# Performance work log

Hardware: AMD Instinct MI355X
Metric: run time of the kernel (lower is better)

Reference implementation:

```python
import jax, jax.numpy as jnp
import numpy as np
from jax import lax

N_CLASS = 21
K_ED = 5
ALPHA = 0.1
BN_EPS = 1e-5


def _conv(x, w):
    # NCHW conv, stride 1, SAME padding
    return lax.conv_general_dilated(x, w, (1, 1), 'SAME',
                                    dimension_numbers=('NCHW', 'OIHW', 'NCHW'))


def _bn(x, g, b, m, v):
    # inference-mode BatchNorm2d with running stats
    scale = (g * lax.rsqrt(v + BN_EPS))[None, :, None, None]
    return (x - m[None, :, None, None]) * scale + b[None, :, None, None]


def _maxpool(x, k):
    return lax.reduce_window(x, -jnp.inf, lax.max, (1, 1, k, k), (1, 1, 1, 1), 'SAME')


def setup_inputs() -> dict:
    key = jax.random.key(0)
    ks = jax.random.split(key, 12)
    N, F, H, W, C = 8, 512, 96, 96, N_CLASS
    feature = jax.random.normal(ks[0], (N, F, H, W), jnp.float32)
    global_pred = jax.random.normal(ks[1], (N, C, H, W), jnp.float32)
    conv1_w = jax.random.normal(ks[2], (256, F, 3, 3), jnp.float32) * 0.02
    bn1_g = jnp.ones((256,), jnp.float32)
    bn1_b = jnp.zeros((256,), jnp.float32)
    bn1_m = jax.random.normal(ks[3], (256,), jnp.float32) * 0.1
    bn1_v = jax.random.uniform(ks[4], (256,), jnp.float32, 0.5, 1.5)
    conv2_w = jax.random.normal(ks[5], (128, 256, 3, 3), jnp.float32) * 0.02
    bn2_g = jnp.ones((128,), jnp.float32)
    bn2_b = jnp.zeros((128,), jnp.float32)
    bn2_m = jax.random.normal(ks[6], (128,), jnp.float32) * 0.1
    bn2_v = jax.random.uniform(ks[7], (128,), jnp.float32, 0.5, 1.5)
    conv3_w = jax.random.normal(ks[8], (C, 128, 1, 1), jnp.float32) * 0.02
    conv3_b = jnp.zeros((C,), jnp.float32)
    return dict(feature=feature, global_pred=global_pred,
                conv1_w=conv1_w, bn1_g=bn1_g, bn1_b=bn1_b, bn1_m=bn1_m, bn1_v=bn1_v,
                conv2_w=conv2_w, bn2_g=bn2_g, bn2_b=bn2_b, bn2_m=bn2_m, bn2_v=bn2_v,
                conv3_w=conv3_w, conv3_b=conv3_b)


def reference(feature, global_pred, conv1_w, bn1_g, bn1_b, bn1_m, bn1_v,
              conv2_w, bn2_g, bn2_b, bn2_m, bn2_v, conv3_w, conv3_b):
    N, F, H, W = feature.shape
    # hard labels -> one-hot [N, C, H, W]
    lbl = jnp.argmax(global_pred, axis=1)
    onehot = jnp.transpose(jax.nn.one_hot(lbl, N_CLASS, dtype=feature.dtype), (0, 3, 1, 2))
    # binary morphology: dilation = max-pool, erosion = -max-pool(-x)
    d = _maxpool(onehot, K_ED)
    e = -_maxpool(-onehot, K_ED)
    transition = jnp.sum(d - e, axis=1, keepdims=True)
    transition = jnp.where(transition >= 1.0, 1.0, transition)  # [N,1,H,W]
    tfeat = feature * transition
    # per-class masked mean over ALL H*W pixels (faithful to .mean(dim=2))
    objs = jnp.einsum('nfhw,nchw->ncf', feature, e) / (H * W)  # [N,C,F]
    # cdist(p=2) between transition-feature pixels and class prototypes
    x = tfeat.reshape(N, F, H * W).transpose(0, 2, 1)  # [N,HW,F]
    x2 = jnp.sum(x * x, axis=-1, keepdims=True)
    o2 = jnp.sum(objs * objs, axis=-1)
    d2 = jnp.maximum(x2 + o2[:, None, :] - 2.0 * jnp.einsum('npf,ncf->npc', x, objs), 0.0)
    cd = jnp.where(d2 > 0, jnp.sqrt(jnp.where(d2 > 0, d2, 1.0)), 0.0)  # safe sqrt
    dist = 1.0 - jax.nn.softmax(cd, axis=-1)  # [N,HW,C]
    obj_feat = jnp.einsum('npc,ncf->nfp', dist, objs).reshape(N, F, H, W)
    fusion = (feature * (1.0 - transition)
              + feature * transition * ALPHA
              + obj_feat * transition * (1.0 - ALPHA))
    # fusion_predictor: convBNReLU -> bilinear x2 -> convBNReLU -> 1x1 conv
    h = jax.nn.relu(_bn(_conv(fusion, conv1_w), bn1_g, bn1_b, bn1_m, bn1_v))
    h = jax.image.resize(h, (N, 256, 2 * H, 2 * W), method='bilinear')
    h = jax.nn.relu(_bn(_conv(h, conv2_w), bn2_g, bn2_b, bn2_m, bn2_v))
    logits = _conv(h, conv3_w) + conv3_b[None, :, None, None]
    # eval mode: softmax over classes
    return jax.nn.softmax(logits, axis=1)
```

## Files before the change

### kernel.cpp

```cpp
#include <hip/hip_runtime.h>
#include <cstdint>
#include <cstddef>

typedef __attribute__((ext_vector_type(4))) float f32x4;
typedef __attribute__((ext_vector_type(8))) short short8;

__device__ __forceinline__ float bf2f(unsigned short u) {
  union { unsigned int i; float f; } x; x.i = ((unsigned int)u) << 16; return x.f;
}
__device__ __forceinline__ unsigned short f2bf(float f) {
  union { float f; unsigned int i; } x; x.f = f;
  unsigned int r = x.i + 0x7fffu + ((x.i >> 16) & 1u);
  return (unsigned short)(r >> 16);
}
__device__ __forceinline__ void gload16(unsigned short* lds, const unsigned short* g) {
  __builtin_amdgcn_global_load_lds(
      (const __attribute__((address_space(1))) unsigned int*)g,
      (__attribute__((address_space(3))) unsigned int*)lds, 16, 0, 0);
}

__global__ void k_prepbn(const float* __restrict__ g1, const float* __restrict__ b1,
                         const float* __restrict__ m1, const float* __restrict__ v1,
                         const float* __restrict__ g2, const float* __restrict__ b2,
                         const float* __restrict__ m2, const float* __restrict__ v2,
                         float* __restrict__ s1, float* __restrict__ bb1,
                         float* __restrict__ s2, float* __restrict__ bb2) {
  int i = threadIdx.x;
  if (i < 256) { float s = g1[i] * rsqrtf(v1[i] + 1e-5f); s1[i] = s; bb1[i] = b1[i] - m1[i] * s; }
  if (i < 128) { float s = g2[i] * rsqrtf(v2[i] + 1e-5f); s2[i] = s; bb2[i] = b2[i] - m2[i] * s; }
}

__global__ void k_prepw1(const float* __restrict__ w, unsigned short* __restrict__ wt) {
  int i = blockIdx.x * 256 + threadIdx.x;
  int o = i / 4608, k = i - o * 4608;
  int cblk = k / 288, r = k - cblk * 288;
  int t = r >> 5, cl = r & 31;
  int ci = cblk * 32 + cl;
  int ty = t / 3, tx = t - ty * 3;
  wt[i] = f2bf(w[((o * 512 + ci) * 3 + ty) * 3 + tx]);
}
__global__ void k_prepw2(const float* __restrict__ w, unsigned short* __restrict__ wt) {
  int i = blockIdx.x * 256 + threadIdx.x;
  int o = i / 2304, k = i - o * 2304;
  int cblk = k / 288, r = k - cblk * 288;
  int t = r >> 5, cl = r & 31;
  int ci = cblk * 32 + cl;
  int ty = t / 3, tx = t - ty * 3;
  wt[i] = f2bf(w[((o * 256 + ci) * 3 + ty) * 3 + tx]);
}
__global__ void k_prepw3(const float* __restrict__ w3, unsigned short* __restrict__ w3b) {
  int i = blockIdx.x * 256 + threadIdx.x;
  int c = i >> 7, k = i & 127;
  w3b[i] = (c < 21) ? f2bf(w3[c * 128 + k]) : (unsigned short)0;
}

template <int HP, int WP, int C>
__global__ void k_border(unsigned short* __restrict__ p) {
  const int B = 2 * WP + 2 * (HP - 2);
  const int total = 8 * B * (C / 8);
  int i = blockIdx.x * 256 + threadIdx.x;
  if (i >= total) return;
  const int cg = i % (C / 8);
  int b = i / (C / 8);
  const int n = b / B; b -= n * B;
  int y, x;
  if (b < WP) { y = 0; x = b; }
  else if (b < 2 * WP) { y = HP - 1; x = b - WP; }
  else { int r = b - 2 * WP; y = 1 + (r >> 1); x = (r & 1) ? (WP - 1) : 0; }
  short8 z = {0, 0, 0, 0, 0, 0, 0, 0};
  *(short8*)&p[(((long)n * HP + y) * WP + x) * C + cg * 8] = z;
}

__global__ __launch_bounds__(256)
void k_featT(const float* __restrict__ feat, unsigned short* __restrict__ featT) {
  const int g = blockIdx.x * 256 + threadIdx.x;
  const int n = g / 9216, p = g - n * 9216;
  const int fg0 = blockIdx.y * 16;
  const float* src = feat + (long)n * 512 * 9216 + p;
  unsigned short* dst = featT + ((long)n * 9216 + p) * 512;
  for (int fg = fg0; fg < fg0 + 16; fg++) {
    short8 o;
    #pragma unroll
    for (int j = 0; j < 8; j++) o[j] = (short)f2bf(src[(long)(fg * 8 + j) * 9216]);
    *(short8*)&dst[fg * 8] = o;
  }
}

__global__ void k_labels(const float* __restrict__ gp, signed char* __restrict__ lab) {
  int p = blockIdx.x * 256 + threadIdx.x;
  int n = p / 9216, q = p - n * 9216;
  const float* g = gp + (long)n * 21 * 9216 + q;
  float best = g[0]; int bi = 0;
  #pragma unroll
  for (int c = 1; c < 21; c++) {
    float v = g[(long)c * 9216];
    if (v > best) { best = v; bi = c; }
  }
  lab[p] = (signed char)bi;
}

__global__ void k_em(const signed char* __restrict__ lab, signed char* __restrict__ em) {
  int p = blockIdx.x * 256 + threadIdx.x;
  int n = p / 9216, q = p - n * 9216, y = q / 96, x = q - y * 96;
  const signed char* L = lab + n * 9216;
  signed char l0 = L[q];
  bool uni = true;
  for (int dy = -2; dy <= 2; dy++) {
    int yy = y + dy; if (yy < 0 || yy > 95) continue;
    for (int dx = -2; dx <= 2; dx++) {
      int xx = x + dx; if (xx < 0 || xx > 95) continue;
      uni = uni && (L[yy * 96 + xx] == l0);
    }
  }
  em[p] = uni ? l0 : (signed char)-1;
}

__global__ void k_objs(const float* __restrict__ feat, const signed char* __restrict__ em,
                       float* __restrict__ objs) {
  const int n = blockIdx.y;
  const int wv = threadIdx.x >> 6, lane = threadIdx.x & 63;
  const int f = blockIdx.x * 4 + wv;
  const float* src = feat + ((long)n * 512 + f) * 9216;
  const signed char* e = em + n * 9216;
  float a[21];
  #pragma unroll
  for (int c = 0; c < 21; c++) a[c] = 0.f;
  for (int p = lane; p < 9216; p += 64) {
    float v = src[p];
    int c0 = e[p];
    #pragma unroll
    for (int c = 0; c < 21; c++) a[c] += (c0 == c) ? v : 0.f;
  }
  #pragma unroll
  for (int c = 0; c < 21; c++) {
    #pragma unroll
    for (int off = 32; off; off >>= 1) a[c] += __shfl_down(a[c], off);
  }
  if (lane == 0) {
    #pragma unroll
    for (int c = 0; c < 21; c++) objs[((long)n * 21 + c) * 512 + f] = a[c] * (1.0f / 9216.0f);
  }
}

__global__ void k_o2(const float* __restrict__ objs, float* __restrict__ o2) {
  int nc = blockIdx.x;
  int lane = threadIdx.x;
  const float* o = objs + (long)nc * 512;
  float s = 0.f;
  for (int f = lane; f < 512; f += 64) { float v = o[f]; s += v * v; }
  #pragma unroll
  for (int off = 32; off; off >>= 1) s += __shfl_down(s, off);
  if (lane == 0) o2[nc] = s;
}

__global__ void k_objsbf(const float* __restrict__ objs, unsigned short* __restrict__ oc) {
  int i = blockIdx.x * 256 + threadIdx.x;
  int n = i / (32 * 512); int r = i - n * 32 * 512;
  int c = r >> 9, f = r & 511;
  oc[i] = (c < 21) ? f2bf(objs[((long)n * 21 + c) * 512 + f]) : (unsigned short)0;
}

__global__ __launch_bounds__(256)
void k_dist_mfma(const unsigned short* __restrict__ featT,
                 const unsigned short* __restrict__ objs_c,
                 const float* __restrict__ o2, float* __restrict__ dist) {
  const int n = blockIdx.y;
  const int w = threadIdx.x >> 6, lane = threadIdx.x & 63;
  const int lrow = lane & 15, kg = lane >> 4;
  const int px = blockIdx.x * 64 + w * 16 + lrow;
  const unsigned short* fb = featT + ((long)n * 9216 + px) * 512 + kg * 8;
  const unsigned short* a0p = objs_c + ((long)n * 32 + lrow) * 512 + kg * 8;
  const unsigned short* a1p = a0p + 16 * 512;
  f32x4 acc0 = {0.f, 0.f, 0.f, 0.f}, acc1 = {0.f, 0.f, 0.f, 0.f};
  float x2 = 0.f;
  #pragma unroll
  for (int s = 0; s < 16; s++) {
    const short8 b = *(const short8*)&fb[s * 32];
    const short8 a0 = *(const short8*)&a0p[s * 32];
    const short8 a1 = *(const short8*)&a1p[s * 32];
    acc0 = __builtin_amdgcn_mfma_f32_16x16x32_bf16(a0, b, acc0, 0, 0, 0);
    acc1 = __builtin_amdgcn_mfma_f32_16x16x32_bf16(a1, b, acc1, 0, 0, 0);
    #pragma unroll
    for (int j = 0; j < 8; j++) { float v = bf2f((unsigned short)b[j]); x2 += v * v; }
  }
  x2 += __shfl_xor(x2, 16); x2 += __shfl_xor(x2, 32);
  float cd[8], mx = -1e30f;
  #pragma unroll
  for (int r = 0; r < 4; r++) {
    const int c = kg * 4 + r;
    float d2 = x2 + o2[n * 21 + c] - 2.f * acc0[r];
    cd[r] = sqrtf(fmaxf(d2, 0.f)); mx = fmaxf(mx, cd[r]);
  }
  #pragma unroll
  for (int r = 0; r < 4; r++) {
    const int c = 16 + kg * 4 + r;
    if (c < 21) {
      float d2 = x2 + o2[n * 21 + c] - 2.f * acc1[r];
      cd[4 + r] = sqrtf(fmaxf(d2, 0.f)); mx = fmaxf(mx, cd[4 + r]);
    } else cd[4 + r] = -1e30f;
  }
  mx = fmaxf(mx, __shfl_xor(mx, 16)); mx = fmaxf(mx, __shfl_xor(mx, 32));
  float sum = 0.f;
  #pragma unroll
  for (int k = 0; k < 8; k++) {
    cd[k] = (cd[k] > -1e29f) ? __expf(cd[k] - mx) : 0.f;
    sum += cd[k];
  }
  sum += __shfl_xor(sum, 16); sum += __shfl_xor(sum, 32);
  const float inv = 1.f / sum;
  #pragma unroll
  for (int r = 0; r < 4; r++)
    dist[((long)n * 21 + kg * 4 + r) * 9216 + px] = 1.f - cd[r] * inv;
  #pragma unroll
  for (int r = 0; r < 4; r++) {
    const int c = 16 + kg * 4 + r;
    if (c < 21) dist[((long)n * 21 + c) * 9216 + px] = 1.f - cd[4 + r] * inv;
  }
}

__global__ __launch_bounds__(256)
void k_fusion(const unsigned short* __restrict__ featT, const signed char* __restrict__ em,
              const float* __restrict__ dist, const float* __restrict__ objs,
              unsigned short* __restrict__ fuP) {
  __shared__ float ob[21 * 512];
  __shared__ float dl[64][21];
  __shared__ signed char eml[64];
  const int blk = blockIdx.x;
  const int n = blk / 144;
  const int p0 = (blk - n * 144) * 64;
  const int tid = threadIdx.x;
  for (int i = tid; i < 21 * 512; i += 256) ob[i] = objs[(long)n * 21 * 512 + i];
  for (int i = tid; i < 64 * 21; i += 256) {
    int px = i & 63, c = i >> 6;
    dl[px][c] = dist[((long)n * 21 + c) * 9216 + p0 + px];
  }
  if (tid < 64) eml[tid] = em[n * 9216 + p0 + tid];
  __syncthreads();
  const int px = tid & 63;
  const int fg = (tid >> 6) * 8;
  const int q = p0 + px;
  const int y = q / 96, x = q - y * 96;
  unsigned short* dst = fuP + (((long)n * 98 + y + 1) * 98 + (x + 1)) * 512;
  const bool t = eml[px] < 0;
  const unsigned short* srcT = featT + ((long)n * 9216 + q) * 512;
  for (int f0 = 0; f0 < 512; f0 += 32) {
    short8 o;
    const short8 fvv = *(const short8*)&srcT[f0 + fg];
    #pragma unroll
    for (int j = 0; j < 8; j++) {
      const int f = f0 + fg + j;
      float fv = bf2f((unsigned short)fvv[j]);
      if (t) {
        float of = 0.f;
        #pragma unroll
        for (int c = 0; c < 21; c++) of += dl[px][c] * ob[c * 512 + f];
        fv = 0.1f * fv + 0.9f * of;
      }
      o[j] = (short)f2bf(fv);
    }
    *(short8*)&dst[fg] = o;
    dst += 32;
  }
}

template <int CIN, int NK>
__global__ __launch_bounds__(256)
void conv3x3_gemm(const unsigned short* __restrict__ inP,
                  const unsigned short* __restrict__ wT,
                  const float* __restrict__ scale, const float* __restrict__ bias,
                  unsigned short* __restrict__ out,
                  int Hout, int Wout, int Hp, int Wp, int COUT, int nbN) {
  __shared__ unsigned short ldsA[3][4096];
  __shared__ unsigned short ldsB[3][4096];
  const int tid = threadIdx.x;
  const int chunk = gridDim.x >> 3;
  const int bid = (blockIdx.x & 7) * chunk + (blockIdx.x >> 3);
  const int mb = bid / nbN, nb = bid - mb * nbN;
  const int bm0 = mb * 128, bn0 = nb * 128;
  const int KT = 9 * CIN;
  const int HWo = Hout * Wout;

  const int rA = tid >> 2;
  const int ch8 = (((tid & 3) ^ ((tid >> 3) & 3)) * 8);
  const int m0 = bm0 + rA, m1 = m0 + 64;
  const int n0 = m0 / HWo; const int q0 = m0 - n0 * HWo;
  const int y0 = q0 / Wout, x0 = q0 - y0 * Wout;
  const int n1 = m1 / HWo; const int q1 = m1 - n1 * HWo;
  const int y1 = q1 / Wout, x1 = q1 - y1 * Wout;
  const unsigned short* gA0 = inP + ((long)(n0 * Hp + y0) * Wp + x0) * CIN + ch8;
  const unsigned short* gA1 = inP + ((long)(n1 * Hp + y1) * Wp + x1) * CIN + ch8;
  const unsigned short* gB0 = wT + (long)(bn0 + rA) * KT + ch8;
  const unsigned short* gB1 = wT + (long)(bn0 + rA + 64) * KT + ch8;

  const int lane = tid & 63;
  const int wv = tid >> 6;
  const int wr = wv >> 1, wc = wv & 1;
  const int lrow = lane & 15, kg = lane >> 4;
  const int arow = wr * 64 + lrow;
  const int aoff = arow * 32 + (kg ^ ((arow >> 1) & 3)) * 8;
  const int brow = wc * 64 + lrow;
  const int boff = brow * 32 + (kg ^ ((brow >> 1) & 3)) * 8;

  f32x4 acc[4][4];
  const f32x4 zero = {0.f, 0.f, 0.f, 0.f};
  #pragma unroll
  for (int i = 0; i < 4; i++)
    #pragma unroll
    for (int j = 0; j < 4; j++) acc[i][j] = zero;

  auto stage = [&](int b, int s) {
    const int cblk = s / 9;
    const int t = s - cblk * 9;
    const int ty = t / 3, tx = t - ty * 3;
    const long offA = (long)(ty * Wp + tx) * CIN + cblk * 32;
    gload16(&ldsA[b][tid * 8], gA0 + offA);
    gload16(&ldsA[b][2048 + tid * 8], gA1 + offA);
    const long k0 = (long)s * 32;
    gload16(&ldsB[b][tid * 8], gB0 + k0);
    gload16(&ldsB[b][2048 + tid * 8], gB1 + k0);
  };

  auto kstep = [&](int rd) {
    const unsigned short* A = ldsA[rd];
    const unsigned short* B = ldsB[rd];
    short8 af[4], bfr[4];
    #pragma unroll
    for (int i = 0; i < 4; i++) af[i] = *(const short8*)&A[aoff + i * 512];
    #pragma unroll
    for (int j = 0; j < 4; j++) bfr[j] = *(const short8*)&B[boff + j * 512];
    __builtin_amdgcn_s_setprio(1);
    #pragma unroll
    for (int i = 0; i < 4; i++)
      #pragma unroll
      for (int j = 0; j < 4; j++)
        acc[i][j] = __builtin_amdgcn_mfma_f32_16x16x32_bf16(af[i], bfr[j], acc[i][j], 0, 0, 0);
    __builtin_amdgcn_s_setprio(0);
  };

  stage(0, 0);
  stage(1, 1);
  int rd = 0, prev = 2;
  for (int s = 0; s < NK - 2; ++s) {
    __builtin_amdgcn_s_barrier();
    asm volatile("" ::: "memory");
    stage(prev, s + 2);
    asm volatile("s_waitcnt vmcnt(8)" ::: "memory");
    __builtin_amdgcn_s_barrier();
    asm volatile("" ::: "memory");
    kstep(rd);
    prev = rd; rd = (rd == 2) ? 0 : rd + 1;
  }
  asm volatile("s_waitcnt vmcnt(4)" ::: "memory");
  __builtin_amdgcn_s_barrier();
  asm volatile("" ::: "memory");
  kstep(rd);
  rd = (rd == 2) ? 0 : rd + 1;
  asm volatile("s_waitcnt vmcnt(0)" ::: "memory");
  __builtin_amdgcn_s_barrier();
  asm volatile("" ::: "memory");
  kstep(rd);

  #pragma unroll
  for (int i = 0; i < 4; i++) {
    const int row = bm0 + wr * 64 + i * 16 + kg * 4;
    #pragma unroll
    for (int j = 0; j < 4; j++) {
      const int col = bn0 + wc * 64 + j * 16 + lrow;
      const float sc = scale[col], bi = bias[col];
      #pragma unroll
      for (int r = 0; r < 4; r++) {
        float v = acc[i][j][r] * sc + bi;
        v = v > 0.f ? v : 0.f;
        out[(long)(row + r) * COUT + col] = f2bf(v);
      }
    }
  }
}

__global__ void k_upsample(const unsigned short* __restrict__ h1,
                           unsigned short* __restrict__ h2P) {
  const int idx = blockIdx.x * 256 + threadIdx.x;
  const int c8 = (idx & 31) * 8;
  const int p = idx >> 5;
  const int n = p / 36864; const int rr = p - n * 36864;
  const int Y = rr / 192, X = rr - Y * 192;
  const int ky = Y >> 1, kx = X >> 1;
  int yA, yB, xA, xB; float wyA, wyB, wxA, wxB;
  if ((Y & 1) == 0) { yA = ky > 0 ? ky - 1 : 0; yB = ky; wyA = 0.25f; wyB = 0.75f; }
  else { yA = ky; yB = ky < 95 ? ky + 1 : 95; wyA = 0.75f; wyB = 0.25f; }
  if ((X & 1) == 0) { xA = kx > 0 ? kx - 1 : 0; xB = kx; wxA = 0.25f; wxB = 0.75f; }
  else { xA = kx; xB = kx < 95 ? kx + 1 : 95; wxA = 0.75f; wxB = 0.25f; }
  const unsigned short* hb = h1 + (long)n * 96 * 96 * 256 + c8;
  const short8 vaa = *(const short8*)&hb[((long)yA * 96 + xA) * 256];
  const short8 vab = *(const short8*)&hb[((long)yA * 96 + xB) * 256];
  const short8 vba = *(const short8*)&hb[((long)yB * 96 + xA) * 256];
  const short8 vbb = *(const short8*)&hb[((long)yB * 96 + xB) * 256];
  short8 o;
  #pragma unroll
  for (int j = 0; j < 8; j++) {
    float v = wyA * (wxA * bf2f((unsigned short)vaa[j]) + wxB * bf2f((unsigned short)vab[j])) +
              wyB * (wxA * bf2f((unsigned short)vba[j]) + wxB * bf2f((unsigned short)vbb[j]));
    o[j] = (short)f2bf(v);
  }
  *(short8*)&h2P[(((long)n * 194 + Y + 1) * 194 + X + 1) * 256 + c8] = o;
}

__global__ __launch_bounds__(256)
void k_conv3_mfma(const unsigned short* __restrict__ h3,
                  const unsigned short* __restrict__ w3b,
                  const float* __restrict__ b3, float* __restrict__ out) {
  const int w = threadIdx.x >> 6, lane = threadIdx.x & 63;
  const int lrow = lane & 15, kg = lane >> 4;
  const long m = (long)blockIdx.x * 64 + w * 16 + lrow;
  const unsigned short* bp = h3 + m * 128 + kg * 8;
  const unsigned short* a0p = w3b + lrow * 128 + kg * 8;
  const unsigned short* a1p = a0p + 16 * 128;
  f32x4 acc0 = {0.f, 0.f, 0.f, 0.f}, acc1 = {0.f, 0.f, 0.f, 0.f};
  #pragma unroll
  for (int s = 0; s < 4; s++) {
    const short8 b = *(const short8*)&bp[s * 32];
    const short8 a0 = *(const short8*)&a0p[s * 32];
    const short8 a1 = *(const short8*)&a1p[s * 32];
    acc0 = __builtin_amdgcn_mfma_f32_16x16x32_bf16(a0, b, acc0, 0, 0, 0);
    acc1 = __builtin_amdgcn_mfma_f32_16x16x32_bf16(a1, b, acc1, 0, 0, 0);
  }
  float lg[8], mx = -1e30f;
  #pragma unroll
  for (int r = 0; r < 4; r++) {
    lg[r] = acc0[r] + b3[kg * 4 + r];
    mx = fmaxf(mx, lg[r]);
  }
  #pragma unroll
  for (int r = 0; r < 4; r++) {
    const int c = 16 + kg * 4 + r;
    if (c < 21) { lg[4 + r] = acc1[r] + b3[c]; mx = fmaxf(mx, lg[4 + r]); }
    else lg[4 + r] = -1e30f;
  }
  mx = fmaxf(mx, __shfl_xor(mx, 16)); mx = fmaxf(mx, __shfl_xor(mx, 32));
  float sum = 0.f;
  #pragma unroll
  for (int k = 0; k < 8; k++) {
    lg[k] = (lg[k] > -1e29f) ? __expf(lg[k] - mx) : 0.f;
    sum += lg[k];
  }
  sum += __shfl_xor(sum, 16); sum += __shfl_xor(sum, 32);
  const float inv = 1.f / sum;
  const int n = (int)(m / 36864);
  const int q = (int)(m - (long)n * 36864);
  #pragma unroll
  for (int r = 0; r < 4; r++)
    out[((long)n * 21 + kg * 4 + r) * 36864 + q] = lg[r] * inv;
  #pragma unroll
  for (int r = 0; r < 4; r++) {
    const int c = 16 + kg * 4 + r;
    if (c < 21) out[((long)n * 21 + c) * 36864 + q] = lg[4 + r] * inv;
  }
}

extern "C" void kernel_launch(void* const* d_in, const int* in_sizes, int n_in,
                              void* d_out, int out_size, void* d_ws, size_t ws_size,
                              hipStream_t stream) {
  const float* feature = (const float*)d_in[0];
  const float* gp = (const float*)d_in[1];
  const float* w1 = (const float*)d_in[2];
  const float* g1 = (const float*)d_in[3];
  const float* b1 = (const float*)d_in[4];
  const float* m1 = (const float*)d_in[5];
  const float* v1 = (const float*)d_in[6];
  const float* w2 = (const float*)d_in[7];
  const float* g2 = (const float*)d_in[8];
  const float* b2 = (const float*)d_in[9];
  const float* m2 = (const float*)d_in[10];
  const float* v2 = (const float*)d_in[11];
  const float* w3 = (const float*)d_in[12];
  const float* b3 = (const float*)d_in[13];
  float* out = (float*)d_out;

  char* ws = (char*)d_ws;
  size_t off = 0;
  auto alloc = [&](size_t bytes) -> void* {
    void* p = ws + off;
    off += (bytes + 255) & ~(size_t)255;
    return p;
  };
  signed char* lab = (signed char*)alloc(73728);
  signed char* em = (signed char*)alloc(73728);
  float* objs = (float*)alloc(8 * 21 * 512 * 4);
  float* o2 = (float*)alloc(168 * 4);
  unsigned short* objs_c = (unsigned short*)alloc((size_t)8 * 32 * 512 * 2);
  float* dist = (float*)alloc((size_t)8 * 21 * 9216 * 4);
  unsigned short* w1t = (unsigned short*)alloc((size_t)256 * 4608 * 2);
  unsigned short* w2t = (unsigned short*)alloc((size_t)128 * 2304 * 2);
  unsigned short* w3b = (unsigned short*)alloc((size_t)32 * 128 * 2);
  float* s1 = (float*)alloc(256 * 4);
  float* bb1 = (float*)alloc(256 * 4);
  float* s2 = (float*)alloc(128 * 4);
  float* bb2 = (float*)alloc(128 * 4);
  const size_t fuP_bytes = (size_t)8 * 98 * 98 * 512 * 2;
  unsigned short* fuP = (unsigned short*)alloc(fuP_bytes);
  const size_t h1_bytes = (size_t)8 * 96 * 96 * 256 * 2;
  unsigned short* h1 = (unsigned short*)alloc(h1_bytes);
  const size_t h2P_bytes = (size_t)8 * 194 * 194 * 256 * 2;
  unsigned short* h2P = (unsigned short*)alloc(h2P_bytes);
  unsigned short* h3 = fuP;
  unsigned short* featT = h2P;

  if (off > ws_size) return;

  k_prepbn<<<1, 256, 0, stream>>>(g1, b1, m1, v1, g2, b2, m2, v2, s1, bb1, s2, bb2);
  k_prepw1<<<4608, 256, 0, stream>>>(w1, w1t);
  k_prepw2<<<1152, 256, 0, stream>>>(w2, w2t);
  k_prepw3<<<16, 256, 0, stream>>>(w3, w3b);

  k_border<98, 98, 512><<<777, 256, 0, stream>>>(fuP);

  k_labels<<<288, 256, 0, stream>>>(gp, lab);
  k_em<<<288, 256, 0, stream>>>(lab, em);
  k_featT<<<dim3(288, 4), 256, 0, stream>>>(feature, featT);
  k_objs<<<dim3(128, 8), 256, 0, stream>>>(feature, em, objs);
  k_o2<<<168, 64, 0, stream>>>(objs, o2);
  k_objsbf<<<512, 256, 0, stream>>>(objs, objs_c);
  k_dist_mfma<<<dim3(144, 8), 256, 0, stream>>>(featT, objs_c, o2, dist);
  k_fusion<<<1152, 256, 0, stream>>>(featT, em, dist, objs, fuP);

  conv3x3_gemm<512, 144><<<1152, 256, 0, stream>>>(fuP, w1t, s1, bb1, h1,
                                                   96, 96, 98, 98, 256, 2);
  k_border<194, 194, 256><<<772, 256, 0, stream>>>(h2P);
  k_upsample<<<36864, 256, 0, stream>>>(h1, h2P);
  conv3x3_gemm<256, 72><<<2304, 256, 0, stream>>>(h2P, w2t, s2, bb2, h3,
                                                  192, 192, 194, 194, 128, 1);
  k_conv3_mfma<<<4608, 256, 0, stream>>>(h3, w3b, b3, out);
}
```

Measured before the change: 869.2 us.

## Compute class prototypes from bf16 transposed features and restructure conv pipeline loop

Replaces the per-feature-channel prototype reduction over fp32 NCHW features with a per-pixel-tile kernel that reads the already-transposed bf16 features. It accumulates into shared memory with atomics and then atomically adds into a zeroed global buffer. This halves the bytes read and avoids the 21-way select loop per pixel, at the cost of bf16 precision in the prototype sums and of atomics. The conv GEMM main loop is also reordered so each stage waits, computes, then issues the next prefetch after the compute, which changes the overlap between loads and MFMA.

```diff
diff --git a/kernel.cpp b/kernel.cpp
--- a/kernel.cpp
+++ b/kernel.cpp
@@ -115,30 +115,34 @@
   em[p] = uni ? l0 : (signed char)-1;
 }
 
-__global__ void k_objs(const float* __restrict__ feat, const signed char* __restrict__ em,
-                       float* __restrict__ objs) {
-  const int n = blockIdx.y;
-  const int wv = threadIdx.x >> 6, lane = threadIdx.x & 63;
-  const int f = blockIdx.x * 4 + wv;
-  const float* src = feat + ((long)n * 512 + f) * 9216;
-  const signed char* e = em + n * 9216;
-  float a[21];
-  #pragma unroll
-  for (int c = 0; c < 21; c++) a[c] = 0.f;
-  for (int p = lane; p < 9216; p += 64) {
-    float v = src[p];
-    int c0 = e[p];
-    #pragma unroll
-    for (int c = 0; c < 21; c++) a[c] += (c0 == c) ? v : 0.f;
-  }
-  #pragma unroll
-  for (int c = 0; c < 21; c++) {
-    #pragma unroll
-    for (int off = 32; off; off >>= 1) a[c] += __shfl_down(a[c], off);
-  }
-  if (lane == 0) {
-    #pragma unroll
-    for (int c = 0; c < 21; c++) objs[((long)n * 21 + c) * 512 + f] = a[c] * (1.0f / 9216.0f);
+__global__ __launch_bounds__(256)
+void k_objsT(const unsigned short* __restrict__ featT, const signed char* __restrict__ em,
+             float* __restrict__ objs) {
+  __shared__ float part[21 * 512];
+  __shared__ signed char emL[256];
+  __shared__ int pres[21];
+  const int b = blockIdx.x;
+  const int n = b / 36;
+  const int px0 = (b - n * 36) * 256;
+  const int tid = threadIdx.x;
+  for (int i = tid; i < 21 * 512; i += 256) part[i] = 0.f;
+  if (tid < 21) pres[tid] = 0;
+  emL[tid] = em[n * 9216 + px0 + tid];
+  __syncthreads();
+  const unsigned short* base = featT + ((long)n * 9216 + px0) * 512 + tid * 2;
+  for (int px = 0; px < 256; px++) {
+    const int c0 = emL[px];
+    if (c0 >= 0) {
+      if (tid == 0) pres[c0] = 1;
+      unsigned int v = *(const unsigned int*)&base[(long)px * 512];
+      atomicAdd(&part[c0 * 512 + tid * 2], bf2f((unsigned short)(v & 0xffff)));
+      atomicAdd(&part[c0 * 512 + tid * 2 + 1], bf2f((unsigned short)(v >> 16)));
+    }
+  }
+  __syncthreads();
+  for (int i = tid; i < 21 * 512; i += 256) {
+    const int c = i >> 9;
+    if (pres[c]) atomicAdd(&objs[(long)n * 21 * 512 + i], part[i] * (1.0f / 9216.0f));
   }
 }
 
@@ -339,26 +343,18 @@
 
   stage(0, 0);
   stage(1, 1);
-  int rd = 0, prev = 2;
-  for (int s = 0; s < NK - 2; ++s) {
-    __builtin_amdgcn_s_barrier();
-    asm volatile("" ::: "memory");
-    stage(prev, s + 2);
-    asm volatile("s_waitcnt vmcnt(8)" ::: "memory");
+  int rd = 0;
+  for (int s = 0; s < NK; ++s) {
+    if (s < NK - 1)
+      asm volatile("s_waitcnt vmcnt(6)" ::: "memory");
+    else
+      asm volatile("s_waitcnt vmcnt(0)" ::: "memory");
     __builtin_amdgcn_s_barrier();
     asm volatile("" ::: "memory");
     kstep(rd);
-    prev = rd; rd = (rd == 2) ? 0 : rd + 1;
-  }
-  asm volatile("s_waitcnt vmcnt(4)" ::: "memory");
-  __builtin_amdgcn_s_barrier();
-  asm volatile("" ::: "memory");
-  kstep(rd);
-  rd = (rd == 2) ? 0 : rd + 1;
-  asm volatile("s_waitcnt vmcnt(0)" ::: "memory");
-  __builtin_amdgcn_s_barrier();
-  asm volatile("" ::: "memory");
-  kstep(rd);
+    if (s + 2 < NK) stage((rd + 2 >= 3) ? rd - 1 : rd + 2, s + 2);
+    rd = (rd == 2) ? 0 : rd + 1;
+  }
 
   #pragma unroll
   for (int i = 0; i < 4; i++) {
@@ -513,11 +509,12 @@
   k_prepw3<<<16, 256, 0, stream>>>(w3, w3b);
 
   k_border<98, 98, 512><<<777, 256, 0, stream>>>(fuP);
+  hipMemsetAsync(objs, 0, 8 * 21 * 512 * 4, stream);
 
   k_labels<<<288, 256, 0, stream>>>(gp, lab);
   k_em<<<288, 256, 0, stream>>>(lab, em);
   k_featT<<<dim3(288, 4), 256, 0, stream>>>(feature, featT);
-  k_objs<<<dim3(128, 8), 256, 0, stream>>>(feature, em, objs);
+  k_objsT<<<288, 256, 0, stream>>>(featT, em, objs);
   k_o2<<<168, 64, 0, stream>>>(objs, o2);
   k_objsbf<<<512, 256, 0, stream>>>(objs, objs_c);
   k_dist_mfma<<<dim3(144, 8), 256, 0, stream>>>(featT, objs_c, o2, dist);
```

New measurement: 796.5 us. -8.4%, faster.
